# Kernel tuning notes

Hardware: AMD Instinct MI355X
Metric: run time of the kernel (lower is better)

Reference implementation:

```python
import jax, jax.numpy as jnp
from jax import lax
import numpy as np

B, N = 131072, 80


def _continuant(a, bc):
    """Three-term complex continuant recursion with shift z = 1j.

    theta_0 = 1, theta_1 = a[0] - i,
    theta_{k+1} = (a[k] - i) * theta_k - bc[k-1] * theta_{k-1}.
    a: (B, N) real, bc: (B, N-1) real. Returns real/imag parts, each (B, N+1).
    """
    Bn, Nn = a.shape
    th0_r = jnp.ones((Bn,), a.dtype)
    th0_i = jnp.zeros((Bn,), a.dtype)
    th1_r = a[:, 0]
    th1_i = -jnp.ones((Bn,), a.dtype)  # imag part of (a0 - i)

    def step(carry, x):
        pr, pim, cr, ci = carry  # theta_{k-1}, theta_k
        ak, bck = x
        # (a_k - i) * theta_k  - bc * theta_{k-1}
        nr = ak * cr + ci - bck * pr
        ni = ak * ci - cr - bck * pim
        return (cr, ci, nr, ni), (nr, ni)

    xs = (a[:, 1:].T, bc.T)  # (N-1, B)
    _, (yr, yi) = lax.scan(step, (th0_r, th0_i, th1_r, th1_i), xs)
    th_r = jnp.concatenate([th0_r[:, None], th1_r[:, None], yr.T], axis=1)
    th_i = jnp.concatenate([th0_i[:, None], th1_i[:, None], yi.T], axis=1)
    return th_r, th_i  # (B, N+1)


def setup_inputs() -> dict:
    key = jax.random.key(0)
    k1, = jax.random.split(key, 1)
    # shift so that a = h0_diag + he ~ 0, keeping the continuants finite in fp32
    he_diag = 2.0 + 0.1 * jax.random.normal(k1, (B, N), dtype=jnp.float32)
    h0_diag = jnp.full((N,), -2.0, dtype=jnp.float32)
    h0_sub = jnp.ones((N - 1,), dtype=jnp.float32)
    h0_super = jnp.ones((N - 1,), dtype=jnp.float32)
    return {"he_diag": he_diag, "h0_diag": h0_diag, "h0_sub": h0_sub, "h0_super": h0_super}


def reference(he_diag, h0_diag, h0_sub, h0_super):
    a = h0_diag[None, :] + he_diag                      # (B, N) effective diagonal
    Bn, Nn = a.shape
    bc = jnp.broadcast_to((h0_super * h0_sub)[None, :], (Bn, Nn - 1))
    # forward (theta) continuants: theta[0..N]
    th_r, th_i = _continuant(a, bc)
    # backward (phi) continuants: phi[i] = continuant of rows i..N-1, phi[N] = 1.
    # phi reversed is the same recursion on flipped a / bc.
    pr_rev, pi_rev = _continuant(a[:, ::-1], bc[:, ::-1])
    phi_r = pr_rev[:, ::-1]   # (B, N+1), phi_r[:, N] == 1
    phi_i = pi_rev[:, ::-1]
    # diagonal Green's function: G_ii = theta_i * phi_{i+1} / theta_N
    num_r = th_r[:, :Nn] * phi_r[:, 1:] - th_i[:, :Nn] * phi_i[:, 1:]
    num_i = th_r[:, :Nn] * phi_i[:, 1:] + th_i[:, :Nn] * phi_r[:, 1:]
    dr = th_r[:, Nn:]
    di = th_i[:, Nn:]
    inv_den = 1.0 / (dr * dr + di * di)   # avoid den**2 overflow in fp32
    g_r = (num_r * dr + num_i * di) * inv_den
    g_i = (num_i * dr - num_r * di) * inv_den
    return jnp.stack([g_r, g_i], axis=-1)  # (B, N, 2) real/imag features
```

## Files before the change

### kernel.cpp

```cpp
#include <hip/hip_runtime.h>

#define MAXN 128

template<int N>
__global__ __launch_bounds__(64, 4) void greens_cf1w(
    const float* __restrict__ he,
    const float* __restrict__ h0d,
    const float* __restrict__ h0sub,
    const float* __restrict__ h0sup,
    float2* __restrict__ out)
{
    constexpr int ROWS = 32;
    constexpr int MID  = N / 2;
    static_assert(N == 80, "tuned for N=80");

    __shared__ float  sA[ROWS][N + 1];
    __shared__ float2 sO[ROWS][17];
    __shared__ float  sBC[N];

    const int t = threadIdx.x;
    if (t < N - 1)      sBC[t]      = h0sub[t] * h0sup[t];
    if (t + 64 < N - 1) sBC[t + 64] = h0sub[t + 64] * h0sup[t + 64];

    const int row0 = blockIdx.x * ROWS;
    const float* __restrict__ tile  = he  + (size_t)row0 * N;
    float2*      __restrict__ otile = out + (size_t)row0 * N;

    #pragma unroll
    for (int i = 0; i < (ROWS * N / 4) / 64; ++i) {
        int idx = i * 64 + t;
        int rr  = idx / (N / 4);
        int q   = idx - rr * (N / 4);
        int col = q * 4;
        float4 v  = *(const float4*)(tile + (size_t)rr * N + col);
        float4 dv = *(const float4*)(h0d + col);
        sA[rr][col + 0] = v.x + dv.x;
        sA[rr][col + 1] = v.y + dv.y;
        sA[rr][col + 2] = v.z + dv.z;
        sA[rr][col + 3] = v.w + dv.w;
    }
    __syncthreads();

    const int  r   = t & 31;
    const bool isA = (t < 32);

    float str_[MID - 1], sti_[MID - 1];
    float2 X;
    X = make_float2(sA[r][isA ? 0 : (N - 1)], -1.0f);

    #pragma unroll
    for (int s = 0; s < MID - 1; ++s) {
        int col = isA ? (s + 1) : (N - 2 - s);
        int bci = isA ? s : (N - 2 - s);
        float inv  = __builtin_amdgcn_rcpf(X.x * X.x + X.y * X.y);
        float binv = sBC[bci] * inv;
        float ex =  binv * X.x;
        float ey = -binv * X.y;
        str_[s] = ex; sti_[s] = ey;
        X.x = sA[r][col] - ex;
        X.y = -1.0f - ey;
    }

    X.x = __shfl_xor(X.x, 32);
    X.y = __shfl_xor(X.y, 32);

    #pragma unroll
    for (int b8 = 0; b8 < 5; ++b8) {
        #pragma unroll
        for (int u = 0; u < 8; ++u) {
            const int u2  = b8 * 8 + u;
            const int j   = isA ? (MID - 1 - u2) : (MID + u2);
            const int bci = isA ? (MID - 1 - u2) : (MID - 1 + u2);
            float inv  = __builtin_amdgcn_rcpf(X.x * X.x + X.y * X.y);
            float binv = sBC[bci] * inv;
            float tx =  binv * X.x;
            float ty = -binv * X.y;
            float a  = sA[r][j];
            float Xx = a - tx;
            float Xy = -1.0f - ty;
            float ox = (u2 < MID - 1) ? str_[MID - 2 - u2] : 0.0f;
            float oy = (u2 < MID - 1) ? sti_[MID - 2 - u2] : 0.0f;
            float zx = Xx - ox;
            float zy = Xy - oy;
            float gi = __builtin_amdgcn_rcpf(zx * zx + zy * zy);
            const int slot = isA ? (j & 7) : (8 + (j & 7));
            sO[r][slot] = make_float2(zx * gi, -zy * gi);
            X.x = Xx; X.y = Xy;
        }
        #pragma unroll
        for (int i = 0; i < 4; ++i) {
            int idx = i * 64 + t;
            int rr  = idx >> 3;
            int u   = idx & 7;
            int col = (u < 4) ? (MID - 8 - 8 * b8 + 2 * u)
                              : (MID - 8 + 8 * b8 + 2 * u);
            float2 g0 = sO[rr][2 * u];
            float2 g1 = sO[rr][2 * u + 1];
            *(float4*)(otile + (size_t)rr * N + col) =
                make_float4(g0.x, g0.y, g1.x, g1.y);
        }
    }
}

__global__ __launch_bounds__(256) void greens_generic(
    const float* __restrict__ he,
    const float* __restrict__ h0d,
    const float* __restrict__ h0sub,
    const float* __restrict__ h0sup,
    float2* __restrict__ out,
    int Bn, int N)
{
    __shared__ float sa[MAXN];
    __shared__ float sbc[MAXN];
    const int t = threadIdx.x;
    if (t < N)     sa[t]  = h0d[t];
    if (t < N - 1) sbc[t] = h0sub[t] * h0sup[t];
    __syncthreads();

    const int b = blockIdx.x * blockDim.x + t;
    if (b >= Bn) return;

    const float* __restrict__ row  = he  + (size_t)b * N;
    float2*      __restrict__ orow = out + (size_t)b * N;

    double tpr = 1.0, tpi = 0.0;
    double tcr = (double)sa[0] + (double)row[0];
    double tci = -1.0;
    orow[0] = make_float2(1.0f, 0.0f);
    for (int k = 1; k < N; ++k) {
        orow[k] = make_float2((float)tcr, (float)tci);
        double ak = (double)sa[k] + (double)row[k];
        double bk = (double)sbc[k - 1];
        double nr = fma(ak, tcr,  tci) - bk * tpr;
        double ni = fma(ak, tci, -tcr) - bk * tpi;
        tpr = tcr; tpi = tci; tcr = nr; tci = ni;
    }
    const double dr = tcr, di = tci;
    const double inv = 1.0 / (dr * dr + di * di);
    const double cr  =  dr * inv;
    const double ci_ = -di * inv;

    double f1r = 1.0, f1i = 0.0;
    double f2r = 0.0, f2i = 0.0;
    for (int j = N - 1; j >= 0; --j) {
        float2 thv = orow[j];
        double tr = (double)thv.x, ti = (double)thv.y;
        double nr = tr * f1r - ti * f1i;
        double ni = tr * f1i + ti * f1r;
        orow[j] = make_float2((float)(nr * cr - ni * ci_),
                              (float)(nr * ci_ + ni * cr));
        double aj = (double)sa[j] + (double)row[j];
        double bj = (j < N - 1) ? (double)sbc[j] : 0.0;
        double pr = fma(aj, f1r,  f1i) - bj * f2r;
        double pi = fma(aj, f1i, -f1r) - bj * f2i;
        f2r = f1r; f2i = f1i; f1r = pr; f1i = pi;
    }
}

extern "C" void kernel_launch(void* const* d_in, const int* in_sizes, int n_in,
                              void* d_out, int out_size, void* d_ws, size_t ws_size,
                              hipStream_t stream) {
    const float* he    = (const float*)d_in[0];
    const float* h0d   = (const float*)d_in[1];
    const float* h0sub = (const float*)d_in[2];
    const float* h0sup = (const float*)d_in[3];
    const int N  = in_sizes[1];
    const int Bn = in_sizes[0] / N;
    float2* out = (float2*)d_out;

    if (N == 80 && (Bn % 32) == 0) {
        const int grid = Bn / 32;
        hipLaunchKernelGGL((greens_cf1w<80>), dim3(grid), dim3(64), 0, stream,
                           he, h0d, h0sub, h0sup, out);
    } else {
        const int block = 256;
        const int grid  = (Bn + block - 1) / block;
        hipLaunchKernelGGL(greens_generic, dim3(grid), dim3(block), 0, stream,
                           he, h0d, h0sub, h0sup, out, Bn, N);
    }
}
```

Before: 127.5 us.

## Preload each thread's half-row into registers and alias output staging onto sA

Each thread now loads its 40 diagonal values into a register array once, using paired float2 LDS reads with the order mirrored for the backward half. The forward and backward recurrences then read those registers instead of issuing per-step LDS loads. The LDS tile is padded to 84 floats so it can be filled with float4 stores, and the output staging buffer reuses the sA storage, which cuts LDS per block. The launch-bounds occupancy hint drops from 4 to 3 to leave room for the extra registers, which may lower occupancy in exchange for fewer LDS round trips in the serial recurrence.

```diff
diff --git a/kernel.cpp b/kernel.cpp
--- a/kernel.cpp
+++ b/kernel.cpp
@@ -3,7 +3,7 @@
 #define MAXN 128
 
 template<int N>
-__global__ __launch_bounds__(64, 4) void greens_cf1w(
+__global__ __launch_bounds__(64, 3) void greens_cf1w(
     const float* __restrict__ he,
     const float* __restrict__ h0d,
     const float* __restrict__ h0sub,
@@ -12,11 +12,11 @@
 {
     constexpr int ROWS = 32;
     constexpr int MID  = N / 2;
+    constexpr int LDA  = 84;
     static_assert(N == 80, "tuned for N=80");
 
-    __shared__ float  sA[ROWS][N + 1];
-    __shared__ float2 sO[ROWS][17];
-    __shared__ float  sBC[N];
+    __shared__ float sA[ROWS][LDA];
+    __shared__ float sBC[N];
 
     const int t = threadIdx.x;
     if (t < N - 1)      sBC[t]      = h0sub[t] * h0sup[t];
@@ -34,36 +34,45 @@
         int col = q * 4;
         float4 v  = *(const float4*)(tile + (size_t)rr * N + col);
         float4 dv = *(const float4*)(h0d + col);
-        sA[rr][col + 0] = v.x + dv.x;
-        sA[rr][col + 1] = v.y + dv.y;
-        sA[rr][col + 2] = v.z + dv.z;
-        sA[rr][col + 3] = v.w + dv.w;
+        *(float4*)&sA[rr][col] =
+            make_float4(v.x + dv.x, v.y + dv.y, v.z + dv.z, v.w + dv.w);
     }
     __syncthreads();
 
     const int  r   = t & 31;
     const bool isA = (t < 32);
 
+    float aR[MID];
+    {
+        const float2* rowp = (const float2*)&sA[r][0];
+        #pragma unroll
+        for (int k = 0; k < MID / 2; ++k) {
+            float2 p = rowp[isA ? k : (MID / 2 - 1 - k + MID / 2)];
+            aR[2 * k]     = isA ? p.x : p.y;
+            aR[2 * k + 1] = isA ? p.y : p.x;
+        }
+    }
+    asm volatile("s_waitcnt lgkmcnt(0)" ::: "memory");
+
     float str_[MID - 1], sti_[MID - 1];
-    float2 X;
-    X = make_float2(sA[r][isA ? 0 : (N - 1)], -1.0f);
+    float2 X = make_float2(aR[0], -1.0f);
 
     #pragma unroll
     for (int s = 0; s < MID - 1; ++s) {
-        int col = isA ? (s + 1) : (N - 2 - s);
         int bci = isA ? s : (N - 2 - s);
         float inv  = __builtin_amdgcn_rcpf(X.x * X.x + X.y * X.y);
         float binv = sBC[bci] * inv;
         float ex =  binv * X.x;
         float ey = -binv * X.y;
         str_[s] = ex; sti_[s] = ey;
-        X.x = sA[r][col] - ex;
+        X.x = aR[s + 1] - ex;
         X.y = -1.0f - ey;
     }
 
     X.x = __shfl_xor(X.x, 32);
     X.y = __shfl_xor(X.y, 32);
 
+    float2 (*sO)[17] = reinterpret_cast<float2(*)[17]>(&sA[0][0]);
     #pragma unroll
     for (int b8 = 0; b8 < 5; ++b8) {
         #pragma unroll
@@ -71,12 +80,12 @@
             const int u2  = b8 * 8 + u;
             const int j   = isA ? (MID - 1 - u2) : (MID + u2);
             const int bci = isA ? (MID - 1 - u2) : (MID - 1 + u2);
+            const int ak  = MID - 1 - u2;
             float inv  = __builtin_amdgcn_rcpf(X.x * X.x + X.y * X.y);
             float binv = sBC[bci] * inv;
             float tx =  binv * X.x;
             float ty = -binv * X.y;
-            float a  = sA[r][j];
-            float Xx = a - tx;
+            float Xx = aR[ak] - tx;
             float Xy = -1.0f - ty;
             float ox = (u2 < MID - 1) ? str_[MID - 2 - u2] : 0.0f;
             float oy = (u2 < MID - 1) ? sti_[MID - 2 - u2] : 0.0f;
```

After: 176.0 us. 38.0% more time.
